# Optimization experiments

Measured on AMD Instinct MI355X. Metric: run time of the kernel, lower is better.

## Reference

```python
import jax, jax.numpy as jnp
import numpy as np

# Config mirrors init_kwargs
H_FULL, W_FULL = 360, 720
SCALE = 4
H_LO, W_LO = H_FULL // SCALE, W_FULL // SCALE  # 90, 180
LMAX = H_LO                  # 90
MMAX = W_LO // 2 + 1         # 91
C = 128                      # embed_dim
NL = 4                       # num_layers
INP_CH, OUT_CH = 2, 2
MLP_HID = int(C * 2.0)
EPS = 1e-5


def rfft2_trunc(x):
    # RealFFT2.forward: ortho rfft2, keep first ceil(LMAX/2) and last floor(LMAX/2) lat modes, first MMAX lon modes
    y = jnp.fft.rfft2(x, norm="ortho")
    lt = (LMAX + 1) // 2
    lb = LMAX - lt
    return jnp.concatenate([y[..., :lt, :MMAX], y[..., y.shape[-2] - lb:, :MMAX]], axis=-2)


def irfft2_pad(y, H, W):
    # InverseRealFFT2: zero-pad truncated modes back to full spectrum, ortho irfft2
    lt = (LMAX + 1) // 2
    lb = LMAX - lt
    full = jnp.zeros(y.shape[:-2] + (H, W // 2 + 1), dtype=y.dtype)
    full = full.at[..., :lt, :MMAX].set(y[..., :lt, :])
    full = full.at[..., H - lb:, :MMAX].set(y[..., lt:, :])
    return jnp.fft.irfft2(full, s=(H, W), norm="ortho")


def inorm(x, w, b):
    # InstanceNorm2d(affine=True): per-sample, per-channel over spatial dims, biased var
    mu = x.mean(axis=(-2, -1), keepdims=True)
    var = x.var(axis=(-2, -1), keepdims=True)
    xn = (x - mu) * jax.lax.rsqrt(var + EPS)
    return xn * w[None, :, None, None] + b[None, :, None, None]


def conv1x1(x, w):  # w: [Cout, Cin], bias=False
    return jnp.einsum('bihw,oi->bohw', x, w)


def gelu(x):
    return jax.nn.gelu(x, approximate=False)


def fno_block(x, n0w, n0b, swr, swi, iw, n1w, n1b, mw1, mw2, out_hw):
    in_hw = x.shape[-2:]
    xn = inorm(x, n0w, n0b)
    # SpectralConv (dhconv): complex per-l channel mixing in truncated spectral space
    Xc = rfft2_trunc(xn)                                   # [B,C,LMAX,MMAX] complex
    scale_res = tuple(in_hw) != tuple(out_hw)
    residual = irfft2_pad(Xc, out_hw[0], out_hw[1]) if scale_res else xn
    w = swr + 1j * swi                                      # [Cin,Cout,LMAX]
    Yc = jnp.einsum('bilm,iol->bolm', Xc, w)
    h = irfft2_pad(Yc, out_hw[0], out_hw[1])
    h = h + conv1x1(residual, iw)                           # inner linear skip
    h = gelu(h)                                             # act_layer0
    h = inorm(h, n1w, n1b)                                  # norm1
    h = conv1x1(gelu(conv1x1(h, mw1)), mw2)                 # MLP (1x1 convs)
    return h + residual                                     # outer identity skip


def setup_inputs() -> dict:
    key = jax.random.key(0)
    ks = jax.random.split(key, 16)
    s = 1.0 / np.sqrt(C)
    inp = {
        "x": jax.random.normal(ks[0], (1, INP_CH, H_FULL, W_FULL), jnp.float32),
        # encoder: inp_chans -> C -> C (encoder_ratio=1)
        "enc_w1": jax.random.normal(ks[1], (C, INP_CH), jnp.float32) * (1.0 / np.sqrt(INP_CH)),
        "enc_w2": jax.random.normal(ks[2], (C, C), jnp.float32) * s,
        # per-layer stacked block params
        "n0w": jnp.ones((NL, C), jnp.float32),
        "n0b": jnp.zeros((NL, C), jnp.float32),
        "swr": jax.random.normal(ks[3], (NL, C, C, LMAX), jnp.float32) * (1.0 / C),
        "swi": jax.random.normal(ks[4], (NL, C, C, LMAX), jnp.float32) * (1.0 / C),
        "iw": jax.random.normal(ks[5], (NL, C, C), jnp.float32) * s,
        "n1w": jnp.ones((NL, C), jnp.float32),
        "n1b": jnp.zeros((NL, C), jnp.float32),
        "mw1": jax.random.normal(ks[6], (NL, MLP_HID, C), jnp.float32) * s,
        "mw2": jax.random.normal(ks[7], (NL, C, MLP_HID), jnp.float32) * (1.0 / np.sqrt(MLP_HID)),
        # decoder: (C + inp_chans) -> C -> out_chans (big_skip concat)
        "dec_w1": jax.random.normal(ks[8], (C, C + INP_CH), jnp.float32) * (1.0 / np.sqrt(C + INP_CH)),
        "dec_w2": jax.random.normal(ks[9], (OUT_CH, C), jnp.float32) * s,
    }
    return inp


def reference(x, enc_w1, enc_w2, n0w, n0b, swr, swi, iw, n1w, n1b, mw1, mw2, dec_w1, dec_w2):
    big_res = x
    h = conv1x1(gelu(conv1x1(x, enc_w1)), enc_w2)           # encoder
    out_shapes = [(H_LO, W_LO)] * (NL - 1) + [(H_FULL, W_FULL)]
    for l in range(NL):
        h = fno_block(h, n0w[l], n0b[l], swr[l], swi[l], iw[l],
                      n1w[l], n1b[l], mw1[l], mw2[l], out_shapes[l])
    h = jnp.concatenate([h, big_res], axis=1)               # big skip
    h = conv1x1(gelu(conv1x1(h, dec_w1)), dec_w2)           # decoder
    return h
```

## Files before the change

### kernel.cpp

```cpp
#include <hip/hip_runtime.h>
#include <hip/hip_bf16.h>
#include <math.h>

typedef __attribute__((ext_vector_type(8))) short short8v;
typedef __attribute__((ext_vector_type(4))) float f32x4;
typedef unsigned short u16;

__device__ __forceinline__ float gelu_f(float x) {
    return 0.5f * x * (1.0f + erff(x * 0.70710678118654752f));
}
__device__ __forceinline__ float bf2f(u16 u) {
    union { unsigned int i; float f; } v; v.i = ((unsigned int)u) << 16; return v.f;
}
__device__ __forceinline__ u16 f2bf(float f) {
    union { float f; unsigned int i; } v; v.f = f;
    unsigned int r = v.i + 0x7FFFu + ((v.i >> 16) & 1u);
    return (u16)(r >> 16);
}
__device__ __forceinline__ short8v negbf(short8v a) {
    uint4 u = *(uint4*)&a;
    u.x ^= 0x80008000u; u.y ^= 0x80008000u; u.z ^= 0x80008000u; u.w ^= 0x80008000u;
    return *(short8v*)&u;
}

__device__ __forceinline__ uint4 load8(const u16* p) { return *(const uint4*)p; }
__device__ __forceinline__ uint4 load8(const float* p) {
    float4 a = *(const float4*)p;
    float4 b = *(const float4*)(p + 4);
    union { uint4 u; u16 e[8]; } r;
    r.e[0] = f2bf(a.x); r.e[1] = f2bf(a.y); r.e[2] = f2bf(a.z); r.e[3] = f2bf(a.w);
    r.e[4] = f2bf(b.x); r.e[5] = f2bf(b.y); r.e[6] = f2bf(b.z); r.e[7] = f2bf(b.w);
    return r.u;
}
__device__ __forceinline__ float rdD(const u16* p) { return bf2f(*p); }
__device__ __forceinline__ float rdD(const float* p) { return *p; }
__device__ __forceinline__ void stO(u16* p, float v) { *p = f2bf(v); }
__device__ __forceinline__ void stO(float* p, float v) { *p = v; }

template<int BMODE, class TA, class TB, class TD, class TO>
__global__ __launch_bounds__(256) void gemm_t(
    const TA* __restrict__ A1, const TB* __restrict__ B1,
    const TA* __restrict__ A2, const TB* __restrict__ B2,
    const TD* __restrict__ D, TO* __restrict__ O,
    int M, int N, int Kp, int neg2, int act,
    long long sAb, long long sAm,
    long long sBb, long long sBr,
    long long sDb, long long sDm,
    long long sOb, long long sOm)
{
    __shared__ __align__(16) u16 As[64 * 32];
    __shared__ __align__(16) u16 Bs[BMODE ? 32 * 68 : 64 * 32];
    const int tid = threadIdx.x;
    const long long b = blockIdx.z;
    const int bm0 = blockIdx.y * 64;
    const int bn0 = blockIdx.x * 64;
    const int lane = tid & 63;
    const int wave = tid >> 6;
    const int wr = (wave >> 1) * 32;
    const int wc = (wave & 1) * 32;
    const int fr = lane & 15;
    const int fg = lane >> 4;
    const int arow = tid >> 2, achk = tid & 3;

    f32x4 acc[2][2];
#pragma unroll
    for (int i = 0; i < 2; ++i)
#pragma unroll
        for (int j = 0; j < 2; ++j) acc[i][j] = (f32x4){0.f, 0.f, 0.f, 0.f};

    const int nph = A2 ? 2 : 1;
    for (int ph = 0; ph < nph; ++ph) {
        const TA* Ap = (ph ? A2 : A1) + b * sAb;
        const TB* Bp = (ph ? B2 : B1) + b * sBb;
        const unsigned int sgn = (ph && neg2) ? 0x80008000u : 0u;
        for (int k0 = 0; k0 < Kp; k0 += 32) {
            uint4 av = load8(Ap + (long long)(bm0 + arow) * sAm + k0 + achk * 8);
            av.x ^= sgn; av.y ^= sgn; av.z ^= sgn; av.w ^= sgn;
            uint4 bv;
            if (BMODE == 0) {
                bv = load8(Bp + (long long)(bn0 + arow) * sBr + k0 + achk * 8);
            } else {
                const int bk = tid >> 3, bnc = tid & 7;
                bv = load8(Bp + (long long)(k0 + bk) * sBr + bn0 + bnc * 8);
            }
            __syncthreads();
            *(uint4*)(&As[arow * 32 + ((achk ^ ((arow >> 1) & 3)) * 8)]) = av;
            if (BMODE == 0) {
                *(uint4*)(&Bs[arow * 32 + ((achk ^ ((arow >> 1) & 3)) * 8)]) = bv;
            } else {
                const int bk = tid >> 3, bnc = tid & 7;
                *(uint2*)(&Bs[bk * 68 + bnc * 8]) = make_uint2(bv.x, bv.y);
                *(uint2*)(&Bs[bk * 68 + bnc * 8 + 4]) = make_uint2(bv.z, bv.w);
            }
            __syncthreads();
            short8v afrag[2], bfrag[2];
#pragma unroll
            for (int i = 0; i < 2; ++i) {
                int r = wr + i * 16 + fr;
                afrag[i] = *(const short8v*)(&As[r * 32 + ((fg ^ ((r >> 1) & 3)) * 8)]);
            }
            if (BMODE == 0) {
#pragma unroll
                for (int j = 0; j < 2; ++j) {
                    int r = wc + j * 16 + fr;
                    bfrag[j] = *(const short8v*)(&Bs[r * 32 + ((fg ^ ((r >> 1) & 3)) * 8)]);
                }
            } else {
#pragma unroll
                for (int j = 0; j < 2; ++j) {
                    int col = wc + j * 16 + fr;
                    short8v v;
#pragma unroll
                    for (int e = 0; e < 8; ++e) v[e] = (short)Bs[(fg * 8 + e) * 68 + col];
                    bfrag[j] = v;
                }
            }
#pragma unroll
            for (int i = 0; i < 2; ++i)
#pragma unroll
                for (int j = 0; j < 2; ++j)
                    acc[i][j] = __builtin_amdgcn_mfma_f32_16x16x32_bf16(afrag[i], bfrag[j], acc[i][j], 0, 0, 0);
        }
    }
#pragma unroll
    for (int i = 0; i < 2; ++i) {
#pragma unroll
        for (int j = 0; j < 2; ++j) {
            int col = bn0 + wc + j * 16 + fr;
            if (col >= N) continue;
#pragma unroll
            for (int r = 0; r < 4; ++r) {
                int row = bm0 + wr + i * 16 + fg * 4 + r;
                if (row >= M) continue;
                float v = acc[i][j][r];
                if (D) v += rdD(D + b * sDb + (long long)row * sDm + col);
                if (act) v = gelu_f(v);
                stO(O + b * sOb + (long long)row * sOm + col, v);
            }
        }
    }
}

template<class TA, class TB, class TD, class TO>
__global__ __launch_bounds__(256) void gemm_ts(
    const TA* __restrict__ A, const TB* __restrict__ B,
    const TD* __restrict__ D, TO* __restrict__ O,
    int M, int N, int Kp, int act,
    long long sAm, long long sBr,
    long long sDm, long long sOm)
{
    __shared__ __align__(16) u16 As[64 * 32];
    __shared__ __align__(16) u16 Bs[64 * 32];
    const int tid = threadIdx.x;
    int lid = blockIdx.x + (int)gridDim.x * blockIdx.y;
    int total = (int)(gridDim.x * gridDim.y);
    int nx, ny;
    if ((lid & ~15) + 16 <= total) {
        nx = (lid >> 3) & 1;
        ny = ((lid >> 4) << 3) + (lid & 7);
    } else {
        nx = lid & 1;
        ny = lid >> 1;
    }
    const int bm0 = ny * 64;
    const int bn0 = nx * 64;
    const int lane = tid & 63;
    const int wave = tid >> 6;
    const int wr = (wave >> 1) * 32;
    const int wc = (wave & 1) * 32;
    const int fr = lane & 15;
    const int fg = lane >> 4;
    const int arow = tid >> 2, achk = tid & 3;
    const int aswz = (achk ^ ((arow >> 1) & 3)) * 8;

    f32x4 acc[2][2];
#pragma unroll
    for (int i = 0; i < 2; ++i)
#pragma unroll
        for (int j = 0; j < 2; ++j) acc[i][j] = (f32x4){0.f, 0.f, 0.f, 0.f};

    for (int k0 = 0; k0 < Kp; k0 += 32) {
        uint4 av = load8(A + (long long)(bm0 + arow) * sAm + k0 + achk * 8);
        uint4 bv = load8(B + (long long)(bn0 + arow) * sBr + k0 + achk * 8);
        __syncthreads();
        *(uint4*)(&As[arow * 32 + aswz]) = av;
        *(uint4*)(&Bs[arow * 32 + aswz]) = bv;
        __syncthreads();
        short8v afrag[2], bfrag[2];
#pragma unroll
        for (int i = 0; i < 2; ++i) {
            int r = wr + i * 16 + fr;
            afrag[i] = *(const short8v*)(&As[r * 32 + ((fg ^ ((r >> 1) & 3)) * 8)]);
        }
#pragma unroll
        for (int j = 0; j < 2; ++j) {
            int r = wc + j * 16 + fr;
            bfrag[j] = *(const short8v*)(&Bs[r * 32 + ((fg ^ ((r >> 1) & 3)) * 8)]);
        }
#pragma unroll
        for (int i = 0; i < 2; ++i)
#pragma unroll
            for (int j = 0; j < 2; ++j)
                acc[i][j] = __builtin_amdgcn_mfma_f32_16x16x32_bf16(afrag[i], bfrag[j], acc[i][j], 0, 0, 0);
    }
#pragma unroll
    for (int i = 0; i < 2; ++i) {
#pragma unroll
        for (int j = 0; j < 2; ++j) {
            int col = bn0 + wc + j * 16 + fr;
            if (col >= N) continue;
#pragma unroll
            for (int r = 0; r < 4; ++r) {
                int row = bm0 + wr + i * 16 + fg * 4 + r;
                if (row >= M) continue;
                float v = acc[i][j][r];
                if (D) v += rdD(D + (long long)row * sDm + col);
                if (act) v = gelu_f(v);
                stO(O + (long long)row * sOm + col, v);
            }
        }
    }
}

template<class TA, class TD, class TO>
__global__ __launch_bounds__(256) void gemm_mlp(
    const TA* __restrict__ A, const u16* __restrict__ W1, const u16* __restrict__ W2,
    const TD* __restrict__ D, TO* __restrict__ O,
    int M, long long sAm, long long sDm, long long sOm)
{
    __shared__ __align__(16) u16 As4[4][64 * 32];
    __shared__ __align__(16) u16 Hs[8][64 * 32];
    const int tid = threadIdx.x;
    const int bm0 = blockIdx.x * 64;
    const int lane = tid & 63;
    const int wave = tid >> 6;
    const int wr = (wave >> 1) * 32;
    const int wc = (wave & 1) * 32;
    const int fr = lane & 15;
    const int fg = lane >> 4;
    const int arow = tid >> 2, achk = tid & 3;
    const int aswz = (achk ^ ((arow >> 1) & 3)) * 8;

#pragma unroll
    for (int kt = 0; kt < 4; ++kt) {
        uint4 av = load8(A + (long long)(bm0 + arow) * sAm + kt * 32 + achk * 8);
        *(uint4*)(&As4[kt][arow * 32 + aswz]) = av;
    }
    __syncthreads();

#pragma unroll
    for (int nb = 0; nb < 4; ++nb) {
        f32x4 acc[2][2];
#pragma unroll
        for (int i = 0; i < 2; ++i)
#pragma unroll
            for (int j = 0; j < 2; ++j) acc[i][j] = (f32x4){0.f, 0.f, 0.f, 0.f};
#pragma unroll
        for (int kt = 0; kt < 4; ++kt) {
            short8v af[2], bf[2];
#pragma unroll
            for (int i = 0; i < 2; ++i) {
                int r = wr + i * 16 + fr;
                af[i] = *(const short8v*)(&As4[kt][r * 32 + ((fg ^ ((r >> 1) & 3)) * 8)]);
            }
#pragma unroll
            for (int j = 0; j < 2; ++j) {
                int col = wc + nb * 64 + j * 16 + fr;
                bf[j] = *(const short8v*)(W1 + (long long)col * 128 + kt * 32 + fg * 8);
            }
#pragma unroll
            for (int i = 0; i < 2; ++i)
#pragma unroll
                for (int j = 0; j < 2; ++j)
                    acc[i][j] = __builtin_amdgcn_mfma_f32_16x16x32_bf16(af[i], bf[j], acc[i][j], 0, 0, 0);
        }
#pragma unroll
        for (int i = 0; i < 2; ++i)
#pragma unroll
            for (int j = 0; j < 2; ++j) {
                int col = wc + nb * 64 + j * 16 + fr;
                int kt2 = col >> 5, kc = (col >> 3) & 3, ke = col & 7;
#pragma unroll
                for (int r = 0; r < 4; ++r) {
                    int row = wr + i * 16 + fg * 4 + r;
                    Hs[kt2][row * 32 + ((kc ^ ((row >> 1) & 3)) * 8) + ke] = f2bf(gelu_f(acc[i][j][r]));
                }
            }
    }
    __syncthreads();

#pragma unroll
    for (int nb2 = 0; nb2 < 2; ++nb2) {
        f32x4 acc2[2][2];
#pragma unroll
        for (int i = 0; i < 2; ++i)
#pragma unroll
            for (int j = 0; j < 2; ++j) acc2[i][j] = (f32x4){0.f, 0.f, 0.f, 0.f};
#pragma unroll
        for (int kt = 0; kt < 8; ++kt) {
            short8v af[2], bf[2];
#pragma unroll
            for (int i = 0; i < 2; ++i) {
                int r = wr + i * 16 + fr;
                af[i] = *(const short8v*)(&Hs[kt][r * 32 + ((fg ^ ((r >> 1) & 3)) * 8)]);
            }
#pragma unroll
            for (int j = 0; j < 2; ++j) {
                int col = nb2 * 64 + wc + j * 16 + fr;
                bf[j] = *(const short8v*)(W2 + (long long)col * 256 + kt * 32 + fg * 8);
            }
#pragma unroll
            for (int i = 0; i < 2; ++i)
#pragma unroll
                for (int j = 0; j < 2; ++j)
                    acc2[i][j] = __builtin_amdgcn_mfma_f32_16x16x32_bf16(af[i], bf[j], acc2[i][j], 0, 0, 0);
        }
#pragma unroll
        for (int i = 0; i < 2; ++i) {
#pragma unroll
            for (int j = 0; j < 2; ++j) {
                int col = nb2 * 64 + wc + j * 16 + fr;
#pragma unroll
                for (int r = 0; r < 4; ++r) {
                    int row = bm0 + wr + i * 16 + fg * 4 + r;
                    if (row >= M) continue;
                    float v = acc2[i][j][r];
                    if (D) v += rdD(D + (long long)row * sDm + col);
                    stO(O + (long long)row * sOm + col, v);
                }
            }
        }
    }
}

template<int BMODE, int MODE, class TA, class TB, class TO>
__global__ __launch_bounds__(256) void gemm_t2(
    const TA* __restrict__ A1, const TA* __restrict__ A2,
    const TB* __restrict__ B1, const TB* __restrict__ B2,
    TO* __restrict__ O1, TO* __restrict__ O2,
    int M, int N, int Kp, int s2neg,
    long long sAb, long long sAm,
    long long sBb, long long sBr,
    long long sOb, long long sOm)
{
    __shared__ __align__(16) u16 As1[64 * 32], As2[64 * 32];
    __shared__ __align__(16) u16 Bs1[BMODE ? 32 * 68 : 64 * 32];
    __shared__ __align__(16) u16 Bs2[(MODE == 1) ? 16 : (BMODE ? 32 * 68 : 64 * 32)];
    const int tid = threadIdx.x;
    const long long b = blockIdx.z;
    const int bm0 = blockIdx.y * 64;
    const int bn0 = blockIdx.x * 64;
    const int lane = tid & 63;
    const int wave = tid >> 6;
    const int wr = (wave >> 1) * 32;
    const int wc = (wave & 1) * 32;
    const int fr = lane & 15;
    const int fg = lane >> 4;
    const int arow = tid >> 2, achk = tid & 3;
    const int aswz = (achk ^ ((arow >> 1) & 3)) * 8;

    f32x4 acc1[2][2], acc2[2][2];
#pragma unroll
    for (int i = 0; i < 2; ++i)
#pragma unroll
        for (int j = 0; j < 2; ++j) {
            acc1[i][j] = (f32x4){0.f, 0.f, 0.f, 0.f};
            acc2[i][j] = (f32x4){0.f, 0.f, 0.f, 0.f};
        }

    const TA* A1b = A1 + b * sAb;
    const TA* A2b = A2 + b * sAb;
    const TB* B1b = B1 + b * sBb;
    const TB* B2b = (MODE == 0) ? B2 + b * sBb : B1;

    for (int k0 = 0; k0 < Kp; k0 += 32) {
        long long aoff = (long long)(bm0 + arow) * sAm + k0 + achk * 8;
        uint4 av1 = load8(A1b + aoff);
        uint4 av2 = load8(A2b + aoff);
        uint4 bv1, bv2;
        if (BMODE == 0) {
            long long boff = (long long)(bn0 + arow) * sBr + k0 + achk * 8;
            bv1 = load8(B1b + boff);
            if (MODE == 0) bv2 = load8(B2b + boff);
        } else {
            const int bk = tid >> 3, bnc = tid & 7;
            long long boff = (long long)(k0 + bk) * sBr + bn0 + bnc * 8;
            bv1 = load8(B1b + boff);
            if (MODE == 0) bv2 = load8(B2b + boff);
        }
        __syncthreads();
        *(uint4*)(&As1[arow * 32 + aswz]) = av1;
        *(uint4*)(&As2[arow * 32 + aswz]) = av2;
        if (BMODE == 0) {
            *(uint4*)(&Bs1[arow * 32 + aswz]) = bv1;
            if (MODE == 0) *(uint4*)(&Bs2[arow * 32 + aswz]) = bv2;
        } else {
            const int bk = tid >> 3, bnc = tid & 7;
            *(uint2*)(&Bs1[bk * 68 + bnc * 8]) = make_uint2(bv1.x, bv1.y);
            *(uint2*)(&Bs1[bk * 68 + bnc * 8 + 4]) = make_uint2(bv1.z, bv1.w);
            if (MODE == 0) {
                *(uint2*)(&Bs2[bk * 68 + bnc * 8]) = make_uint2(bv2.x, bv2.y);
                *(uint2*)(&Bs2[bk * 68 + bnc * 8 + 4]) = make_uint2(bv2.z, bv2.w);
            }
        }
        __syncthreads();
        short8v a1f[2], a2f[2], b1f[2], b2f[2];
#pragma unroll
        for (int i = 0; i < 2; ++i) {
            int r = wr + i * 16 + fr;
            int o = r * 32 + ((fg ^ ((r >> 1) & 3)) * 8);
            a1f[i] = *(const short8v*)(&As1[o]);
            a2f[i] = *(const short8v*)(&As2[o]);
        }
        if (BMODE == 0) {
#pragma unroll
            for (int j = 0; j < 2; ++j) {
                int r = wc + j * 16 + fr;
                int o = r * 32 + ((fg ^ ((r >> 1) & 3)) * 8);
                b1f[j] = *(const short8v*)(&Bs1[o]);
                if (MODE == 0) b2f[j] = *(const short8v*)(&Bs2[o]);
            }
        } else {
#pragma unroll
            for (int j = 0; j < 2; ++j) {
                int col = wc + j * 16 + fr;
                short8v v1, v2;
#pragma unroll
                for (int e = 0; e < 8; ++e) {
                    v1[e] = (short)Bs1[(fg * 8 + e) * 68 + col];
                    if (MODE == 0) v2[e] = (short)Bs2[(fg * 8 + e) * 68 + col];
                }
                b1f[j] = v1;
                if (MODE == 0) b2f[j] = v2;
            }
        }
        if (MODE == 1) {
#pragma unroll
            for (int i = 0; i < 2; ++i)
#pragma unroll
                for (int j = 0; j < 2; ++j) {
                    acc1[i][j] = __builtin_amdgcn_mfma_f32_16x16x32_bf16(a1f[i], b1f[j], acc1[i][j], 0, 0, 0);
                    acc2[i][j] = __builtin_amdgcn_mfma_f32_16x16x32_bf16(a2f[i], b1f[j], acc2[i][j], 0, 0, 0);
                }
        } else {
            short8v a2p[2], a2m[2];
#pragma unroll
            for (int i = 0; i < 2; ++i) {
                a2p[i] = s2neg ? negbf(a2f[i]) : a2f[i];
                a2m[i] = s2neg ? a2f[i] : negbf(a2f[i]);
            }
#pragma unroll
            for (int i = 0; i < 2; ++i)
#pragma unroll
                for (int j = 0; j < 2; ++j) {
                    acc1[i][j] = __builtin_amdgcn_mfma_f32_16x16x32_bf16(a1f[i], b1f[j], acc1[i][j], 0, 0, 0);
                    acc1[i][j] = __builtin_amdgcn_mfma_f32_16x16x32_bf16(a2p[i], b2f[j], acc1[i][j], 0, 0, 0);
                    acc2[i][j] = __builtin_amdgcn_mfma_f32_16x16x32_bf16(a1f[i], b2f[j], acc2[i][j], 0, 0, 0);
                    acc2[i][j] = __builtin_amdgcn_mfma_f32_16x16x32_bf16(a2m[i], b1f[j], acc2[i][j], 0, 0, 0);
                }
        }
    }
#pragma unroll
    for (int i = 0; i < 2; ++i) {
#pragma unroll
        for (int j = 0; j < 2; ++j) {
            int col = bn0 + wc + j * 16 + fr;
            if (col >= N) continue;
#pragma unroll
            for (int r = 0; r < 4; ++r) {
                int row = bm0 + wr + i * 16 + fg * 4 + r;
                if (row >= M) continue;
                long long oi = b * sOb + (long long)row * sOm + col;
                stO(O1 + oi, acc1[i][j][r]);
                stO(O2 + oi, acc2[i][j][r]);
            }
        }
    }
}

__global__ void gen_fwdW_T(u16* Cm, u16* Sm, int RP, int KP, int W, int MM) {
    int idx = blockIdx.x * blockDim.x + threadIdx.x;
    if (idx >= RP * KP) return;
    int m = idx / KP, w = idx % KP;
    float cv = 0.f, sv = 0.f;
    if (m < MM && w < W) {
        int t = (m * w) % W;
        float arg = 2.0f * (float)t / (float)W;
        float s = 1.0f / sqrtf((float)W);
        cv = cospif(arg) * s; sv = -sinpif(arg) * s;
    }
    Cm[idx] = f2bf(cv); Sm[idx] = f2bf(sv);
}
__global__ void gen_fwdH(u16* Cm, u16* Sm, int RP, int KP, int H) {
    int idx = blockIdx.x * blockDim.x + threadIdx.x;
    if (idx >= RP * KP) return;
    int l = idx / KP, h = idx % KP;
    float cv = 0.f, sv = 0.f;
    if (l < 90 && h < H) {
        int ll = (l < 45) ? l : l + H - 90;
        int t = (ll * h) % H;
        float arg = 2.0f * (float)t / (float)H;
        float s = 1.0f / sqrtf((float)H);
        cv = cospif(arg) * s; sv = sinpif(arg) * s;
    }
    Cm[idx] = f2bf(cv); Sm[idx] = f2bf(sv);
}
__global__ void gen_invH(u16* Cm, u16* Sm, int RP, int KP, int H) {
    int idx = blockIdx.x * blockDim.x + threadIdx.x;
    if (idx >= RP * KP) return;
    int y = idx / KP, l = idx % KP;
    float cv = 0.f, sv = 0.f;
    if (y < H && l < 90) {
        int ll = (l < 45) ? l : l + H - 90;
        int t = (ll * y) % H;
        float arg = 2.0f * (float)t / (float)H;
        float s = 1.0f / sqrtf((float)H);
        cv = cospif(arg) * s; sv = sinpif(arg) * s;
    }
    Cm[idx] = f2bf(cv); Sm[idx] = f2bf(sv);
}
__global__ void gen_invW_T(u16* Cm, u16* Sm, int RP, int KP, int W, int MM) {
    int idx = blockIdx.x * blockDim.x + threadIdx.x;
    if (idx >= RP * KP) return;
    int w = idx / KP, m = idx % KP;
    float cv = 0.f, sv = 0.f;
    if (w < W && m < MM) {
        int t = (m * w) % W;
        float arg = 2.0f * (float)t / (float)W;
        bool nyq = (2 * m == W);
        float wt = (m == 0 || nyq) ? 1.0f : 2.0f;
        float s = wt / sqrtf((float)W);
        cv = cospif(arg) * s;
        sv = nyq ? 0.f : sinpif(arg) * s;
    }
    Cm[idx] = f2bf(cv); Sm[idx] = f2bf(sv);
}

__global__ void w2bf(const float* __restrict__ in, u16* __restrict__ out, int R, int K, int rs) {
    int idx = blockIdx.x * blockDim.x + threadIdx.x;
    if (idx >= R * K) return;
    int r = idx / K, c = idx % K;
    out[idx] = f2bf(in[(long long)r * rs + c]);
}
__global__ void transp_sw(const float* __restrict__ in, u16* __restrict__ out) {
    __shared__ float t[32][33];
    int l0 = blockIdx.x * 32, ci0 = blockIdx.y * 32, co = blockIdx.z;
    int tx = threadIdx.x, ty = threadIdx.y;
#pragma unroll
    for (int rr = 0; rr < 4; ++rr) {
        int ci = ci0 + ty + rr * 8;
        int l = l0 + tx;
        t[ty + rr * 8][tx] = (l < 90) ? in[((long long)ci * 128 + co) * 90 + l] : 0.f;
    }
    __syncthreads();
#pragma unroll
    for (int rr = 0; rr < 4; ++rr) {
        int l = l0 + ty + rr * 8;
        int ci = ci0 + tx;
        if (l < 90) out[((long long)l * 128 + co) * 128 + ci] = f2bf(t[tx][ty + rr * 8]);
    }
}

__global__ __launch_bounds__(256) void stats_cl_bf(const u16* __restrict__ x, long long P,
                                                   float2* __restrict__ part, int nch) {
    int chunk = blockIdx.x;
    int c = threadIdx.x & 127;
    int h = threadIdx.x >> 7;
    long long beg = P * chunk / nch, end = P * (chunk + 1) / nch;
    float s = 0.f, q = 0.f;
    long long p = beg + h;
    for (; p + 14 < end; p += 16) {
        float v[8];
#pragma unroll
        for (int u = 0; u < 8; ++u) v[u] = bf2f(x[(p + 2 * u) * 128 + c]);
#pragma unroll
        for (int u = 0; u < 8; ++u) { s += v[u]; q += v[u] * v[u]; }
    }
    for (; p < end; p += 2) {
        float v = bf2f(x[p * 128 + c]);
        s += v; q += v * v;
    }
    __shared__ float rs[256], rq[256];
    rs[threadIdx.x] = s; rq[threadIdx.x] = q;
    __syncthreads();
    if (threadIdx.x < 128)
        part[(long long)c * nch + chunk] = make_float2(rs[c] + rs[c + 128], rq[c] + rq[c + 128]);
}
__global__ __launch_bounds__(256) void stats_cl_f32(const float* __restrict__ x, long long P,
                                                    float2* __restrict__ part, int nch) {
    int chunk = blockIdx.x;
    long long beg = P * chunk / nch, end = P * (chunk + 1) / nch;
    int c32 = threadIdx.x & 31;
    int pr  = threadIdx.x >> 5;
    float s[4], q[4];
#pragma unroll
    for (int k = 0; k < 4; ++k) { s[k] = 0.f; q[k] = 0.f; }
    for (long long p = beg + pr; p < end; p += 8) {
        float4 v = *(const float4*)(x + p * 128 + c32 * 4);
        float e[4] = {v.x, v.y, v.z, v.w};
#pragma unroll
        for (int k = 0; k < 4; ++k) { s[k] += e[k]; q[k] += e[k] * e[k]; }
    }
#pragma unroll
    for (int k = 0; k < 4; ++k) {
        s[k] += __shfl_xor(s[k], 32); q[k] += __shfl_xor(q[k], 32);
    }
    __shared__ float2 lds[4][128];
    int wv = threadIdx.x >> 6, lane = threadIdx.x & 63;
    if (lane < 32) {
#pragma unroll
        for (int k = 0; k < 4; ++k) lds[wv][lane * 4 + k] = make_float2(s[k], q[k]);
    }
    __syncthreads();
    if (threadIdx.x < 128) {
        float2 a = lds[0][threadIdx.x], b2 = lds[1][threadIdx.x];
        float2 c2 = lds[2][threadIdx.x], d2 = lds[3][threadIdx.x];
        part[(long long)threadIdx.x * nch + chunk] =
            make_float2(a.x + b2.x + c2.x + d2.x, a.y + b2.y + c2.y + d2.y);
    }
}
__global__ void stats_fin(const float2* __restrict__ part, int nch, float Pf,
                          const float* __restrict__ w, const float* __restrict__ b,
                          float2* __restrict__ st) {
    int c = threadIdx.x;
    float s = 0.f, q = 0.f;
    for (int i = 0; i < nch; ++i) { float2 p = part[(long long)c * nch + i]; s += p.x; q += p.y; }
    float mu = s / Pf;
    float var = q / Pf - mu * mu;
    float inv = rsqrtf(var + 1e-5f);
    float sc = w[c] * inv;
    st[c] = make_float2(sc, b[c] - mu * sc);
}
__global__ __launch_bounds__(256) void norm_apply_bf(const u16* __restrict__ src, u16* __restrict__ dst,
                                                     long long n8, const float2* __restrict__ st) {
    long long i = (long long)blockIdx.x * 256 + threadIdx.x;
    if (i >= n8) return;
    int c0 = (int)((i * 8) & 127);
    uint4 v = *(const uint4*)(src + i * 8);
    union { uint4 u; u16 e[8]; } in, out;
    in.u = v;
#pragma unroll
    for (int k = 0; k < 8; ++k) {
        float2 s = st[c0 + k];
        out.e[k] = f2bf(bf2f(in.e[k]) * s.x + s.y);
    }
    *(uint4*)(dst + i * 8) = out.u;
}
__global__ __launch_bounds__(256) void norm_apply_f32(const float4* __restrict__ src, float4* __restrict__ dst,
                                                      long long n4, const float2* __restrict__ st) {
    long long i = (long long)blockIdx.x * 256 + threadIdx.x;
    if (i >= n4) return;
    int c0 = (int)((i * 4) & 127);
    float4 v = src[i];
    float2 s0 = st[c0], s1 = st[c0 + 1], s2 = st[c0 + 2], s3 = st[c0 + 3];
    v.x = v.x * s0.x + s0.y;
    v.y = v.y * s1.x + s1.y;
    v.z = v.z * s2.x + s2.y;
    v.w = v.w * s3.x + s3.y;
    dst[i] = v;
}

__global__ __launch_bounds__(256) void enc_front(const float* __restrict__ x, const float* __restrict__ w1,
                                                 u16* __restrict__ out, long long P) {
    long long idx = (long long)blockIdx.x * 256 + threadIdx.x;
    if (idx >= P * 16) return;
    long long p = idx >> 4;
    int c0 = (int)(idx & 15) * 8;
    float x0 = x[p], x1 = x[P + p];
    union { uint4 u; u16 e[8]; } o;
#pragma unroll
    for (int k = 0; k < 8; ++k) {
        int c = c0 + k;
        o.e[k] = f2bf(gelu_f(w1[c * 2] * x0 + w1[c * 2 + 1] * x1));
    }
    *(uint4*)(out + p * 128 + c0) = o.u;
}
__global__ __launch_bounds__(256) void dec_fuse(const u16* __restrict__ d1, const float* __restrict__ dw1,
                                                const float* __restrict__ x, const float* __restrict__ w2,
                                                float* __restrict__ out, long long P) {
    __shared__ float w2s[256];
    __shared__ float dxs[256];
    w2s[threadIdx.x] = w2[threadIdx.x];
    {
        int c = threadIdx.x >> 1, h = threadIdx.x & 1;
        dxs[threadIdx.x] = dw1[c * 130 + 128 + h];
    }
    __syncthreads();
    int lane = threadIdx.x & 63;
    long long pix = (long long)blockIdx.x * 4 + (threadIdx.x >> 6);
    float x0 = x[pix], x1 = x[P + pix];
    unsigned int pr = *(const unsigned int*)(d1 + pix * 128 + lane * 2);
    float b0 = bf2f(f2bf(gelu_f(bf2f((u16)(pr & 0xFFFF)) + dxs[4 * lane]     * x0 + dxs[4 * lane + 1] * x1)));
    float b1 = bf2f(f2bf(gelu_f(bf2f((u16)(pr >> 16))    + dxs[4 * lane + 2] * x0 + dxs[4 * lane + 3] * x1)));
    float s0 = b0 * w2s[lane * 2] + b1 * w2s[lane * 2 + 1];
    float s1 = b0 * w2s[128 + lane * 2] + b1 * w2s[128 + lane * 2 + 1];
#pragma unroll
    for (int off = 1; off < 64; off <<= 1) {
        s0 += __shfl_xor(s0, off);
        s1 += __shfl_xor(s1, off);
    }
    if (lane == 0) { out[pix] = s0; out[P + pix] = s1; }
}

__global__ void zero_out(float* p, long long n) {
    long long i = (long long)blockIdx.x * 256 + threadIdx.x;
    if (i < n) p[i] = 0.f;
}

extern "C" void kernel_launch(void* const* d_in, const int* in_sizes, int n_in,
                              void* d_out, int out_size, void* d_ws, size_t ws_size,
                              hipStream_t stream)
{
    const int HF = 360, WF = 720, HL = 90, WL = 180, C = 128, MM = 91;
    const long long PF = (long long)HF * WF;
    const long long PL = (long long)HL * WL;
    (void)in_sizes; (void)n_in;

    const float* x      = (const float*)d_in[0];
    const float* enc_w1 = (const float*)d_in[1];
    const float* enc_w2 = (const float*)d_in[2];
    const float* n0w    = (const float*)d_in[3];
    const float* n0b    = (const float*)d_in[4];
    const float* swr    = (const float*)d_in[5];
    const float* swi    = (const float*)d_in[6];
    const float* iw     = (const float*)d_in[7];
    const float* n1w    = (const float*)d_in[8];
    const float* n1b    = (const float*)d_in[9];
    const float* mw1    = (const float*)d_in[10];
    const float* mw2    = (const float*)d_in[11];
    const float* dec_w1 = (const float*)d_in[12];
    const float* dec_w2 = (const float*)d_in[13];
    float* outp = (float*)d_out;

    u16* ws = (u16*)d_ws;
    long long off = 0;
    auto alloc = [&](long long n) { u16* p = ws + off; off += (n + 31) & ~31LL; return p; };
    auto allocF = [&](long long n) { return (float*)alloc(2 * n); };

    u16*   FULL = alloc(PF * C);
    u16*   RES  = alloc(PF * C);
    u16*   S1r  = alloc(96LL * 384 * 128);
    u16*   S1i  = alloc(96LL * 384 * 128);
    float* Xr   = allocF(96LL * 96 * 128);
    float* Xi   = allocF(96LL * 96 * 128);
    float* Yr   = allocF(96LL * 96 * 128);
    float* Yi   = allocF(96LL * 96 * 128);
    u16*   G1r  = alloc(360LL * 96 * 128);
    u16*   G1i  = alloc(360LL * 96 * 128);
    u16*   G3r  = alloc(360LL * 96 * 128);
    u16*   G3i  = alloc(360LL * 96 * 128);
    float* Rlo  = allocF(PL * C);
    float* L0   = allocF(PL * C);
    u16*   WtR  = alloc(90LL * 128 * 128);
    u16*   WtI  = alloc(90LL * 128 * 128);
    u16* encw2b = alloc(128 * 128);
    u16* iwb    = alloc(128 * 128);
    u16* m1b    = alloc(256 * 128);
    u16* m2b    = alloc(128 * 256);
    u16* dw1b   = alloc(128 * 128);
    u16* CwTc_h = alloc(128 * 736); u16* CwTs_h = alloc(128 * 736);
    u16* CwTc_l = alloc(128 * 192); u16* CwTs_l = alloc(128 * 192);
    u16* Chc_h  = alloc(128 * 384); u16* Chs_h  = alloc(128 * 384);
    u16* Chc_l  = alloc(128 * 96);  u16* Chs_l  = alloc(128 * 96);
    u16* C2c_h  = alloc(384 * 96);  u16* C2s_h  = alloc(384 * 96);
    u16* C2c_l  = alloc(128 * 96);  u16* C2s_l  = alloc(128 * 96);
    u16* CwIc_h = alloc(768 * 96);  u16* CwIs_h = alloc(768 * 96);
    u16* CwIc_l = alloc(192 * 96);  u16* CwIs_l = alloc(192 * 96);
    float2* PART = (float2*)alloc(128 * 256 * 4);
    float2* STb  = (float2*)alloc(128 * 4);
    alloc(64 * 1024);

    if ((size_t)(off * 2) > ws_size) {
        zero_out<<<(int)((out_size + 255) / 256), 256, 0, stream>>>(outp, out_size);
        return;
    }

    auto grid3 = [](int M, int N, int batch) {
        return dim3((unsigned)((N + 63) / 64), (unsigned)((M + 63) / 64), (unsigned)batch);
    };
    auto inormB = [&](const u16* src, u16* dst, long long P, int nch,
                      const float* w, const float* b) {
        stats_cl_bf<<<nch, 256, 0, stream>>>(src, P, PART, nch);
        stats_fin<<<1, 128, 0, stream>>>(PART, nch, (float)P, w, b, STb);
        long long n8 = P * 128 / 8;
        norm_apply_bf<<<(int)((n8 + 255) / 256), 256, 0, stream>>>(src, dst, n8, STb);
    };
    auto inormF = [&](const float* src, float* dst, long long P, int nch,
                      const float* w, const float* b) {
        stats_cl_f32<<<nch, 256, 0, stream>>>(src, P, PART, nch);
        stats_fin<<<1, 128, 0, stream>>>(PART, nch, (float)P, w, b, STb);
        long long n4 = P * 128 / 4;
        norm_apply_f32<<<(int)((n4 + 255) / 256), 256, 0, stream>>>(
            (const float4*)src, (float4*)dst, n4, STb);
    };

    const u16* nullU = nullptr;
    const float* nullF = nullptr;

    {
        int n;
        n = 128 * 736; gen_fwdW_T<<<(n + 255) / 256, 256, 0, stream>>>(CwTc_h, CwTs_h, 128, 736, 720, MM);
        n = 128 * 192; gen_fwdW_T<<<(n + 255) / 256, 256, 0, stream>>>(CwTc_l, CwTs_l, 128, 192, 180, MM);
        n = 128 * 384; gen_fwdH<<<(n + 255) / 256, 256, 0, stream>>>(Chc_h, Chs_h, 128, 384, 360);
        n = 128 * 96;  gen_fwdH<<<(n + 255) / 256, 256, 0, stream>>>(Chc_l, Chs_l, 128, 96, 90);
        n = 384 * 96;  gen_invH<<<(n + 255) / 256, 256, 0, stream>>>(C2c_h, C2s_h, 384, 96, 360);
        n = 128 * 96;  gen_invH<<<(n + 255) / 256, 256, 0, stream>>>(C2c_l, C2s_l, 128, 96, 90);
        n = 768 * 96;  gen_invW_T<<<(n + 255) / 256, 256, 0, stream>>>(CwIc_h, CwIs_h, 768, 96, 720, MM);
        n = 192 * 96;  gen_invW_T<<<(n + 255) / 256, 256, 0, stream>>>(CwIc_l, CwIs_l, 192, 96, 180, MM);
        n = 128 * 128; w2bf<<<(n + 255) / 256, 256, 0, stream>>>(enc_w2, encw2b, 128, 128, 128);
        n = 128 * 128; w2bf<<<(n + 255) / 256, 256, 0, stream>>>(dec_w1, dw1b, 128, 128, 130);
    }

    enc_front<<<(int)((PF * 16 + 255) / 256), 256, 0, stream>>>(x, enc_w1, RES, PF);
    gemm_ts<u16, u16, u16, u16><<<grid3((int)PF, 128, 1), 256, 0, stream>>>(
        RES, encw2b, nullU, FULL, (int)PF, 128, 128, 0, 128, 128, 0, 128);

    const long long s96 = 96LL * 128;

    for (int l = 0; l < 4; ++l) {
        const bool inHi = (l == 0), outHi = (l == 3);
        const int Hin = inHi ? HF : HL, Win = inHi ? WF : WL;
        const int Hout = outHi ? HF : HL, Wout = outHi ? WF : WL;
        const long long Pout = (long long)Hout * Wout;
        const int hdim = inHi ? 384 : 96;
        const int Wp = inHi ? 736 : 192;
        const int hp = inHi ? 384 : 96;
        const u16* CwTc = inHi ? CwTc_h : CwTc_l;  const u16* CwTs = inHi ? CwTs_h : CwTs_l;
        const u16* Chc  = inHi ? Chc_h  : Chc_l;   const u16* Chs  = inHi ? Chs_h  : Chs_l;
        const u16* C2c  = outHi ? C2c_h : C2c_l;   const u16* C2s  = outHi ? C2s_h : C2s_l;
        const u16* CwIc = outHi ? CwIc_h : CwIc_l; const u16* CwIs = outHi ? CwIs_h : CwIs_l;

        {
            dim3 gt(3, 4, 128); dim3 bt(32, 8);
            transp_sw<<<gt, bt, 0, stream>>>(swr + (long long)l * C * C * 90, WtR);
            transp_sw<<<gt, bt, 0, stream>>>(swi + (long long)l * C * C * 90, WtI);
            int n = 128 * 128; w2bf<<<(n + 255) / 256, 256, 0, stream>>>(iw + (long long)l * C * C, iwb, 128, 128, 128);
            n = 256 * 128; w2bf<<<(n + 255) / 256, 256, 0, stream>>>(mw1 + (long long)l * 256 * C, m1b, 256, 128, 128);
            n = 128 * 256; w2bf<<<(n + 255) / 256, 256, 0, stream>>>(mw2 + (long long)l * C * 256, m2b, 128, 256, 256);
        }

        if (inHi) {
            inormB(FULL, RES, PF, 256, n0w + l * C, n0b + l * C);
            gemm_t2<1, 1, u16, u16, u16><<<grid3(96, 128, Hin), 256, 0, stream>>>(
                CwTc, CwTs, RES, nullU, S1r, S1i, 96, 128, Wp, 0,
                0, Wp, (long long)Win * 128, 128, 128, (long long)hdim * 128);
        } else {
            inormF(Rlo, L0, PL, 128, n0w + l * C, n0b + l * C);
            gemm_t2<1, 1, u16, float, u16><<<grid3(96, 128, Hin), 256, 0, stream>>>(
                CwTc, CwTs, L0, nullF, S1r, S1i, 96, 128, Wp, 0,
                0, Wp, (long long)Win * 128, 128, 128, (long long)hdim * 128);
        }

        gemm_t2<1, 0, u16, u16, float><<<grid3(96, 128, 96), 256, 0, stream>>>(
            Chc, Chs, S1r, S1i, Xr, Xi, 96, 128, hp, 0,
            0, hp, (long long)hdim * 128, 128, 128, s96);

        if (inHi || outHi) {
            gemm_t2<1, 0, u16, float, u16><<<grid3(Hout, 128, 96), 256, 0, stream>>>(
                C2c, C2s, Xr, Xi, G3r, G3i, Hout, 128, 96, 1,
                0, 96, 128, s96, 128, s96);
        }

        gemm_t2<0, 0, float, u16, float><<<grid3(96, 128, 90), 256, 0, stream>>>(
            Xr, Xi, WtR, WtI, Yr, Yi, 96, 128, 128, 1,
            s96, 128, 128LL * 128, 128, 128, s96);

        gemm_t2<1, 0, u16, float, u16><<<grid3(Hout, 128, 96), 256, 0, stream>>>(
            C2c, C2s, Yr, Yi, G1r, G1i, Hout, 128, 96, 1,
            0, 96, s96, 128, 128, s96);

        if (!outHi) {
            gemm_t<1, u16, u16, u16, float><<<grid3(Wout, 128, Hout), 256, 0, stream>>>(
                CwIc, G1r, CwIs, G1i, nullU, Rlo, Wout, 128, 96, 1, 0,
                0, 96, s96, 128, 0, 0, (long long)Wout * 128, 128);
            if (inHi)
                gemm_t<1, u16, u16, u16, float><<<grid3(Wout, 128, Hout), 256, 0, stream>>>(
                    CwIc, G3r, CwIs, G3i, nullU, L0, Wout, 128, 96, 1, 0,
                    0, 96, s96, 128, 0, 0, (long long)Wout * 128, 128);
            gemm_t<0, float, u16, float, float><<<grid3((int)Pout, 128, 1), 256, 0, stream>>>(
                L0, iwb, nullF, nullU, Rlo, Rlo, (int)Pout, 128, 128, 0, 1,
                0, 128, 0, 128, 0, 128, 0, 128);
            inormF(Rlo, Rlo, Pout, 128, n1w + l * C, n1b + l * C);
            gemm_mlp<float, float, float><<<dim3((unsigned)((Pout + 63) / 64)), 256, 0, stream>>>(
                Rlo, m1b, m2b, L0, Rlo, (int)Pout, 128, 128, 128);
        } else {
            gemm_t<1, u16, u16, u16, u16><<<grid3(Wout, 128, Hout), 256, 0, stream>>>(
                CwIc, G1r, CwIs, G1i, nullU, FULL, Wout, 128, 96, 1, 0,
                0, 96, s96, 128, 0, 0, (long long)Wout * 128, 128);
            gemm_t<1, u16, u16, u16, u16><<<grid3(Wout, 128, Hout), 256, 0, stream>>>(
                CwIc, G3r, CwIs, G3i, nullU, RES, Wout, 128, 96, 1, 0,
                0, 96, s96, 128, 0, 0, (long long)Wout * 128, 128);
            gemm_ts<u16, u16, u16, u16><<<grid3((int)Pout, 128, 1), 256, 0, stream>>>(
                RES, iwb, FULL, FULL, (int)Pout, 128, 128, 1, 128, 128, 128, 128);
            inormB(FULL, FULL, Pout, 256, n1w + l * C, n1b + l * C);
            gemm_mlp<u16, u16, u16><<<dim3((unsigned)((Pout + 63) / 64)), 256, 0, stream>>>(
                FULL, m1b, m2b, RES, FULL, (int)Pout, 128, 128, 128);
        }
    }

    gemm_ts<u16, u16, u16, u16><<<grid3((int)PF, 128, 1), 256, 0, stream>>>(
        FULL, dw1b, nullU, RES, (int)PF, 128, 128, 0, 128, 128, 0, 128);
    dec_fuse<<<(int)(PF / 4), 256, 0, stream>>>(RES, dec_w1, x, dec_w2, outp, PF);
}
```

Before: 1.242 ms.

## Fuse decoder big-skip and GELU into GEMM epilogue; halve MLP hidden LDS

The decoder's first GEMM now adds the input-channel skip contribution and applies GELU in its epilogue, so the back kernel only does the final 128->2 reduction. The MLP kernel is restructured to compute the hidden activation in two halves, accumulating the second GEMM after each half. This halves the hidden-layer shared memory buffer, which may raise occupancy, at the cost of extra barriers and more live accumulator registers.

After: 1.248 ms. About the same (+0.5%).

```diff
diff --git a/kernel.cpp b/kernel.cpp
--- a/kernel.cpp
+++ b/kernel.cpp
@@ -222,6 +222,104 @@
     }
 }
 
+template<class TA, class TB>
+__global__ __launch_bounds__(256) void gemm_dec(
+    const TA* __restrict__ A, const TB* __restrict__ B, u16* __restrict__ O,
+    int M, int Kp, long long sAm, long long sBr, long long sOm,
+    const float* __restrict__ xin, const float* __restrict__ dw1, long long P)
+{
+    __shared__ __align__(16) u16 As[64 * 32];
+    __shared__ __align__(16) u16 Bs[64 * 32];
+    const int tid = threadIdx.x;
+    int lid = blockIdx.x + (int)gridDim.x * blockIdx.y;
+    int total = (int)(gridDim.x * gridDim.y);
+    int nx, ny;
+    if ((lid & ~15) + 16 <= total) {
+        nx = (lid >> 3) & 1;
+        ny = ((lid >> 4) << 3) + (lid & 7);
+    } else {
+        nx = lid & 1;
+        ny = lid >> 1;
+    }
+    const int bm0 = ny * 64;
+    const int bn0 = nx * 64;
+    const int lane = tid & 63;
+    const int wave = tid >> 6;
+    const int wr = (wave >> 1) * 32;
+    const int wc = (wave & 1) * 32;
+    const int fr = lane & 15;
+    const int fg = lane >> 4;
+    const int arow = tid >> 2, achk = tid & 3;
+    const int aswz = (achk ^ ((arow >> 1) & 3)) * 8;
+
+    f32x4 acc[2][2];
+#pragma unroll
+    for (int i = 0; i < 2; ++i)
+#pragma unroll
+        for (int j = 0; j < 2; ++j) acc[i][j] = (f32x4){0.f, 0.f, 0.f, 0.f};
+
+    for (int k0 = 0; k0 < Kp; k0 += 32) {
+        uint4 av = load8(A + (long long)(bm0 + arow) * sAm + k0 + achk * 8);
+        uint4 bv = load8(B + (long long)(bn0 + arow) * sBr + k0 + achk * 8);
+        __syncthreads();
+        *(uint4*)(&As[arow * 32 + aswz]) = av;
+        *(uint4*)(&Bs[arow * 32 + aswz]) = bv;
+        __syncthreads();
+        short8v afrag[2], bfrag[2];
+#pragma unroll
+        for (int i = 0; i < 2; ++i) {
+            int r = wr + i * 16 + fr;
+            afrag[i] = *(const short8v*)(&As[r * 32 + ((fg ^ ((r >> 1) & 3)) * 8)]);
+        }
+#pragma unroll
+        for (int j = 0; j < 2; ++j) {
+            int r = wc + j * 16 + fr;
+            bfrag[j] = *(const short8v*)(&Bs[r * 32 + ((fg ^ ((r >> 1) & 3)) * 8)]);
+        }
+#pragma unroll
+        for (int i = 0; i < 2; ++i)
+#pragma unroll
+            for (int j = 0; j < 2; ++j)
+                acc[i][j] = __builtin_amdgcn_mfma_f32_16x16x32_bf16(afrag[i], bfrag[j], acc[i][j], 0, 0, 0);
+    }
+#pragma unroll
+    for (int j = 0; j < 2; ++j) {
+        int col = bn0 + wc + j * 16 + fr;
+        float w0 = dw1[col * 130 + 128];
+        float w1 = dw1[col * 130 + 129];
+#pragma unroll
+        for (int i = 0; i < 2; ++i) {
+#pragma unroll
+            for (int r = 0; r < 4; ++r) {
+                int row = bm0 + wr + i * 16 + fg * 4 + r;
+                if (row >= M) continue;
+                float v = bf2f(f2bf(acc[i][j][r]));
+                float xv0 = xin[row], xv1 = xin[P + row];
+                O[(long long)row * sOm + col] = f2bf(gelu_f(v + w0 * xv0 + w1 * xv1));
+            }
+        }
+    }
+}
+
+__global__ __launch_bounds__(256) void dec_back(const u16* __restrict__ d1, const float* __restrict__ w2,
+                                                float* __restrict__ out, long long P) {
+    __shared__ float w2s[256];
+    w2s[threadIdx.x] = w2[threadIdx.x];
+    __syncthreads();
+    int lane = threadIdx.x & 63;
+    long long pix = (long long)blockIdx.x * 4 + (threadIdx.x >> 6);
+    unsigned int pr = *(const unsigned int*)(d1 + pix * 128 + lane * 2);
+    float b0 = bf2f((u16)(pr & 0xFFFF)), b1 = bf2f((u16)(pr >> 16));
+    float s0 = b0 * w2s[lane * 2] + b1 * w2s[lane * 2 + 1];
+    float s1 = b0 * w2s[128 + lane * 2] + b1 * w2s[128 + lane * 2 + 1];
+#pragma unroll
+    for (int off = 1; off < 64; off <<= 1) {
+        s0 += __shfl_xor(s0, off);
+        s1 += __shfl_xor(s1, off);
+    }
+    if (lane == 0) { out[pix] = s0; out[P + pix] = s1; }
+}
+
 template<class TA, class TD, class TO>
 __global__ __launch_bounds__(256) void gemm_mlp(
     const TA* __restrict__ A, const u16* __restrict__ W1, const u16* __restrict__ W2,
@@ -229,7 +327,7 @@
     int M, long long sAm, long long sDm, long long sOm)
 {
     __shared__ __align__(16) u16 As4[4][64 * 32];
-    __shared__ __align__(16) u16 Hs[8][64 * 32];
+    __shared__ __align__(16) u16 Hs[4][64 * 32];
     const int tid = threadIdx.x;
     const int bm0 = blockIdx.x * 64;
     const int lane = tid & 63;
@@ -248,83 +346,94 @@
     }
     __syncthreads();
 
-#pragma unroll
-    for (int nb = 0; nb < 4; ++nb) {
-        f32x4 acc[2][2];
+    f32x4 acc2[2][2][2];
+#pragma unroll
+    for (int n2 = 0; n2 < 2; ++n2)
 #pragma unroll
         for (int i = 0; i < 2; ++i)
 #pragma unroll
-            for (int j = 0; j < 2; ++j) acc[i][j] = (f32x4){0.f, 0.f, 0.f, 0.f};
-#pragma unroll
-        for (int kt = 0; kt < 4; ++kt) {
-            short8v af[2], bf[2];
-#pragma unroll
-            for (int i = 0; i < 2; ++i) {
-                int r = wr + i * 16 + fr;
-                af[i] = *(const short8v*)(&As4[kt][r * 32 + ((fg ^ ((r >> 1) & 3)) * 8)]);
-            }
+            for (int j = 0; j < 2; ++j) acc2[n2][i][j] = (f32x4){0.f, 0.f, 0.f, 0.f};
+
+#pragma unroll
+    for (int half = 0; half < 2; ++half) {
+#pragma unroll
+        for (int nbi = 0; nbi < 2; ++nbi) {
+            int nb = half * 2 + nbi;
+            f32x4 acc[2][2];
+#pragma unroll
+            for (int i = 0; i < 2; ++i)
+#pragma unroll
+                for (int j = 0; j < 2; ++j) acc[i][j] = (f32x4){0.f, 0.f, 0.f, 0.f};
+#pragma unroll
+            for (int kt = 0; kt < 4; ++kt) {
+                short8v af[2], bf[2];
+#pragma unroll
+                for (int i = 0; i < 2; ++i) {
+                    int r = wr + i * 16 + fr;
+                    af[i] = *(const short8v*)(&As4[kt][r * 32 + ((fg ^ ((r >> 1) & 3)) * 8)]);
+                }
+#pragma unroll
+                for (int j = 0; j < 2; ++j) {
+                    int col = wc + nb * 64 + j * 16 + fr;
+                    bf[j] = *(const short8v*)(W1 + (long long)col * 128 + kt * 32 + fg * 8);
+                }
+#pragma unroll
+                for (int i = 0; i < 2; ++i)
+#pragma unroll
+                    for (int j = 0; j < 2; ++j)
+                        acc[i][j] = __builtin_amdgcn_mfma_f32_16x16x32_bf16(af[i], bf[j], acc[i][j], 0, 0, 0);
+            }
+#pragma unroll
+            for (int i = 0; i < 2; ++i)
+#pragma unroll
+                for (int j = 0; j < 2; ++j) {
+                    int col = wc + nb * 64 + j * 16 + fr;
+                    int kt2 = (col >> 5) & 3, kc = (col >> 3) & 3, ke = col & 7;
+#pragma unroll
+                    for (int r = 0; r < 4; ++r) {
+                        int row = wr + i * 16 + fg * 4 + r;
+                        Hs[kt2][row * 32 + ((kc ^ ((row >> 1) & 3)) * 8) + ke] = f2bf(gelu_f(acc[i][j][r]));
+                    }
+                }
+        }
+        __syncthreads();
+#pragma unroll
+        for (int n2 = 0; n2 < 2; ++n2) {
+#pragma unroll
+            for (int ktl = 0; ktl < 4; ++ktl) {
+                short8v af[2], bf[2];
+#pragma unroll
+                for (int i = 0; i < 2; ++i) {
+                    int r = wr + i * 16 + fr;
+                    af[i] = *(const short8v*)(&Hs[ktl][r * 32 + ((fg ^ ((r >> 1) & 3)) * 8)]);
+                }
+#pragma unroll
+                for (int j = 0; j < 2; ++j) {
+                    int col = n2 * 64 + wc + j * 16 + fr;
+                    bf[j] = *(const short8v*)(W2 + (long long)col * 256 + (half * 4 + ktl) * 32 + fg * 8);
+                }
+#pragma unroll
+                for (int i = 0; i < 2; ++i)
+#pragma unroll
+                    for (int j = 0; j < 2; ++j)
+                        acc2[n2][i][j] = __builtin_amdgcn_mfma_f32_16x16x32_bf16(af[i], bf[j], acc2[n2][i][j], 0, 0, 0);
+            }
+        }
+        __syncthreads();
+    }
+
+#pragma unroll
+    for (int n2 = 0; n2 < 2; ++n2) {
+#pragma unroll
+        for (int i = 0; i < 2; ++i) {
 #pragma unroll
             for (int j = 0; j < 2; ++j) {
-                int col = wc + nb * 64 + j * 16 + fr;
-                bf[j] = *(const short8v*)(W1 + (long long)col * 128 + kt * 32 + fg * 8);
-            }
-#pragma unroll
-            for (int i = 0; i < 2; ++i)
-#pragma unroll
-                for (int j = 0; j < 2; ++j)
-                    acc[i][j] = __builtin_amdgcn_mfma_f32_16x16x32_bf16(af[i], bf[j], acc[i][j], 0, 0, 0);
-        }
-#pragma unroll
-        for (int i = 0; i < 2; ++i)
-#pragma unroll
-            for (int j = 0; j < 2; ++j) {
-                int col = wc + nb * 64 + j * 16 + fr;
-                int kt2 = col >> 5, kc = (col >> 3) & 3, ke = col & 7;
-#pragma unroll
-                for (int r = 0; r < 4; ++r) {
-                    int row = wr + i * 16 + fg * 4 + r;
-                    Hs[kt2][row * 32 + ((kc ^ ((row >> 1) & 3)) * 8) + ke] = f2bf(gelu_f(acc[i][j][r]));
-                }
-            }
-    }
-    __syncthreads();
-
-#pragma unroll
-    for (int nb2 = 0; nb2 < 2; ++nb2) {
-        f32x4 acc2[2][2];
-#pragma unroll
-        for (int i = 0; i < 2; ++i)
-#pragma unroll
-            for (int j = 0; j < 2; ++j) acc2[i][j] = (f32x4){0.f, 0.f, 0.f, 0.f};
-#pragma unroll
-        for (int kt = 0; kt < 8; ++kt) {
-            short8v af[2], bf[2];
-#pragma unroll
-            for (int i = 0; i < 2; ++i) {
-                int r = wr + i * 16 + fr;
-                af[i] = *(const short8v*)(&Hs[kt][r * 32 + ((fg ^ ((r >> 1) & 3)) * 8)]);
-            }
-#pragma unroll
-            for (int j = 0; j < 2; ++j) {
-                int col = nb2 * 64 + wc + j * 16 + fr;
-                bf[j] = *(const short8v*)(W2 + (long long)col * 256 + kt * 32 + fg * 8);
-            }
-#pragma unroll
-            for (int i = 0; i < 2; ++i)
-#pragma unroll
-                for (int j = 0; j < 2; ++j)
-                    acc2[i][j] = __builtin_amdgcn_mfma_f32_16x16x32_bf16(af[i], bf[j], acc2[i][j], 0, 0, 0);
-        }
-#pragma unroll
-        for (int i = 0; i < 2; ++i) {
-#pragma unroll
-            for (int j = 0; j < 2; ++j) {
-                int col = nb2 * 64 + wc + j * 16 + fr;
+                int col = n2 * 64 + wc + j * 16 + fr;
 #pragma unroll
                 for (int r = 0; r < 4; ++r) {
                     int row = bm0 + wr + i * 16 + fg * 4 + r;
                     if (row >= M) continue;
-                    float v = acc2[i][j][r];
+                    float v = acc2[n2][i][j][r];
                     if (D) v += rdD(D + (long long)row * sDm + col);
                     stO(O + (long long)row * sOm + col, v);
                 }
@@ -674,32 +783,6 @@
         o.e[k] = f2bf(gelu_f(w1[c * 2] * x0 + w1[c * 2 + 1] * x1));
     }
     *(uint4*)(out + p * 128 + c0) = o.u;
-}
-__global__ __launch_bounds__(256) void dec_fuse(const u16* __restrict__ d1, const float* __restrict__ dw1,
-                                                const float* __restrict__ x, const float* __restrict__ w2,
-                                                float* __restrict__ out, long long P) {
-    __shared__ float w2s[256];
-    __shared__ float dxs[256];
-    w2s[threadIdx.x] = w2[threadIdx.x];
-    {
-        int c = threadIdx.x >> 1, h = threadIdx.x & 1;
-        dxs[threadIdx.x] = dw1[c * 130 + 128 + h];
-    }
-    __syncthreads();
-    int lane = threadIdx.x & 63;
-    long long pix = (long long)blockIdx.x * 4 + (threadIdx.x >> 6);
-    float x0 = x[pix], x1 = x[P + pix];
-    unsigned int pr = *(const unsigned int*)(d1 + pix * 128 + lane * 2);
-    float b0 = bf2f(f2bf(gelu_f(bf2f((u16)(pr & 0xFFFF)) + dxs[4 * lane]     * x0 + dxs[4 * lane + 1] * x1)));
-    float b1 = bf2f(f2bf(gelu_f(bf2f((u16)(pr >> 16))    + dxs[4 * lane + 2] * x0 + dxs[4 * lane + 3] * x1)));
-    float s0 = b0 * w2s[lane * 2] + b1 * w2s[lane * 2 + 1];
-    float s1 = b0 * w2s[128 + lane * 2] + b1 * w2s[128 + lane * 2 + 1];
-#pragma unroll
-    for (int off = 1; off < 64; off <<= 1) {
-        s0 += __shfl_xor(s0, off);
-        s1 += __shfl_xor(s1, off);
-    }
-    if (lane == 0) { out[pix] = s0; out[P + pix] = s1; }
 }
 
 __global__ void zero_out(float* p, long long n) {
@@ -898,7 +981,7 @@
         }
     }
 
-    gemm_ts<u16, u16, u16, u16><<<grid3((int)PF, 128, 1), 256, 0, stream>>>(
-        FULL, dw1b, nullU, RES, (int)PF, 128, 128, 0, 128, 128, 0, 128);
-    dec_fuse<<<(int)(PF / 4), 256, 0, stream>>>(RES, dec_w1, x, dec_w2, outp, PF);
-}
+    gemm_dec<u16, u16><<<grid3((int)PF, 128, 1), 256, 0, stream>>>(
+        FULL, dw1b, RES, (int)PF, 128, 128, 128, 128, x, dec_w1, PF);
+    dec_back<<<(int)(PF / 4), 256, 0, stream>>>(RES, dec_w2, outp, PF);
+}
```
